# Performance work log

Measured on AMD Instinct MI355X. Metric: run time of the kernel, lower is better.

Reference implementation:

```python
import jax, jax.numpy as jnp
import numpy as np

N, E, D, L, G = 50000, 800000, 128, 3, 64
DIM_OUT = 10
EPS_BN = 1e-5
EPS_AGG = 1e-6


def setup_inputs() -> dict:
    key = jax.random.key(0)
    ks = jax.random.split(key, 10)
    x = jax.random.normal(ks[0], (N, D), jnp.float32)
    edge_attr = jax.random.normal(ks[1], (E, D), jnp.float32)
    edge_index = jax.random.randint(ks[2], (2, E), 0, N)
    batch_vec = jnp.sort(jax.random.randint(ks[3], (N,), 0, G))
    s = 1.0 / np.sqrt(D)
    def w(k, shape):
        return jax.random.uniform(k, shape, jnp.float32, -s, s)
    lin_w = w(ks[4], (L, 4, D, D))   # per-layer stacked A,B,D,E weights
    lin_b = w(ks[5], (L, 4, D))
    bn_gamma = jnp.ones((L, D), jnp.float32)
    bn_beta = jnp.zeros((L, D), jnp.float32)
    post_w1 = w(ks[6], (D, D)); post_b1 = w(ks[7], (D,))
    post_w2 = w(ks[8], (D, DIM_OUT)); post_b2 = w(ks[9], (DIM_OUT,))
    return dict(x=x, edge_attr=edge_attr, edge_index=edge_index, batch_vec=batch_vec,
                lin_w=lin_w, lin_b=lin_b, bn_gamma=bn_gamma, bn_beta=bn_beta,
                post_w1=post_w1, post_b1=post_b1, post_w2=post_w2, post_b2=post_b2)


def _batchnorm_train(h, gamma, beta):
    # training-mode BN over node dim (biased variance, as in torch)
    mu = h.mean(0)
    var = h.var(0)
    return (h - mu) * jax.lax.rsqrt(var + EPS_BN) * gamma + beta


def reference(x, edge_attr, edge_index, batch_vec, lin_w, lin_b, bn_gamma, bn_beta,
              post_w1, post_b1, post_w2, post_b2):
    src, dst = edge_index[0], edge_index[1]   # j -> i (source_to_target)
    e = edge_attr
    for l in range(L):
        x_in = x
        # fused A,B,D,E projections: [4, N, D]
        proj = jnp.einsum('nd,kdo->kno', x, lin_w[l]) + lin_b[l][:, None, :]
        Ax, Bx, Dx, Ex = proj[0], proj[1], proj[2], proj[3]
        e_ij = Dx[dst] + Ex[src]                # [E, D]
        sigma = jax.nn.sigmoid(e_ij)
        num = jax.ops.segment_sum(sigma * Bx[src], dst, num_segments=N)
        den = jax.ops.segment_sum(sigma, dst, num_segments=N)
        h = Ax + num / (den + EPS_AGG)
        h = jax.nn.relu(_batchnorm_train(h, bn_gamma[l], bn_beta[l]))
        x = x_in + h                            # residual
        e = e_ij                                # edge features updated (bn_edge_e unused in forward)
    counts = jax.ops.segment_sum(jnp.ones((N,), x.dtype), batch_vec, num_segments=G)
    pooled = jax.ops.segment_sum(x, batch_vec, num_segments=G) / jnp.maximum(counts, 1.0)[:, None]
    h = jax.nn.relu(pooled @ post_w1 + post_b1)
    return h @ post_w2 + post_b2                # [G, DIM_OUT]
```

## Files before the change

kernel.cpp:

```cpp
#include <hip/hip_runtime.h>
#include <math.h>

constexpr int N_NODES = 50000;
constexpr int N_EDGES = 800000;
constexpr int DIM     = 128;
constexpr int NLAYERS = 3;
constexpr int NGRAPH  = 64;
constexpr int DOUT    = 10;
constexpr float EPS_BN  = 1e-5f;
constexpr float EPS_AGG = 1e-6f;

typedef __attribute__((ext_vector_type(8))) short   bf16x8;
typedef __attribute__((ext_vector_type(4))) float   floatx4;
typedef __attribute__((ext_vector_type(4))) unsigned short ushort4v;

__device__ inline unsigned short f2bf(float f) {
    union { float f; unsigned int u; } v; v.f = f;
    unsigned int u = v.u;
    return (unsigned short)((u + 0x7fffu + ((u >> 16) & 1u)) >> 16);
}
__device__ inline float bf2f(unsigned short h) {
    union { unsigned int u; float f; } v; v.u = ((unsigned int)h) << 16;
    return v.f;
}

__global__ void hist_kernel(const int* __restrict__ dst, int* __restrict__ cnt) {
    int e = blockIdx.x * 256 + threadIdx.x;
    if (e < N_EDGES) atomicAdd(&cnt[dst[e]], 1);
}

__global__ void scan1_kernel(const int* __restrict__ cnt, int* __restrict__ row_ptr,
                             int* __restrict__ partials) {
    __shared__ int s[256];
    int i = blockIdx.x * 256 + threadIdx.x;
    int v = (i < N_NODES) ? cnt[i] : 0;
    s[threadIdx.x] = v;
    __syncthreads();
    for (int off = 1; off < 256; off <<= 1) {
        int t = (threadIdx.x >= off) ? s[threadIdx.x - off] : 0;
        __syncthreads();
        s[threadIdx.x] += t;
        __syncthreads();
    }
    if (i < N_NODES) row_ptr[i] = s[threadIdx.x] - v;
    if (threadIdx.x == 255) partials[blockIdx.x] = s[255];
}

__global__ void scan2_kernel(int* partials, int nb) {
    __shared__ int s[256];
    int t = threadIdx.x;
    int v = (t < nb) ? partials[t] : 0;
    s[t] = v;
    __syncthreads();
    for (int off = 1; off < 256; off <<= 1) {
        int u = (t >= off) ? s[t - off] : 0;
        __syncthreads();
        s[t] += u;
        __syncthreads();
    }
    if (t < nb) partials[t] = s[t] - v;
}

__global__ void scan3_kernel(int* row_ptr, const int* __restrict__ partials) {
    int i = blockIdx.x * 256 + threadIdx.x;
    if (i < N_NODES) row_ptr[i] += partials[blockIdx.x];
    if (blockIdx.x == 0 && threadIdx.x == 0) row_ptr[N_NODES] = N_EDGES;
}

__global__ void scatter_kernel(const int* __restrict__ src, const int* __restrict__ dst,
                               const int* __restrict__ row_ptr, int* __restrict__ cursor,
                               int* __restrict__ col_src) {
    int e = blockIdx.x * 256 + threadIdx.x;
    if (e < N_EDGES) {
        int d = dst[e];
        int pos = row_ptr[d] + atomicAdd(&cursor[d], 1);
        col_src[pos] = src[e];
    }
}

__global__ void wconv_kernel(const float* __restrict__ W, unsigned short* __restrict__ Wt) {
    int idx = blockIdx.x * 256 + threadIdx.x;
    int c = idx & 127, d = (idx >> 7) & 127, lk = idx >> 14;
    Wt[((size_t)lk * 128 + c) * 128 + d] = f2bf(W[idx]);
}

__global__ __launch_bounds__(256) void xinit_kernel(const float* __restrict__ x_in,
                                                    float* __restrict__ x_cur,
                                                    unsigned short* __restrict__ xb) {
    int i4 = blockIdx.x * 256 + threadIdx.x;
    float4 v = *(const float4*)&x_in[(size_t)i4 * 4];
    *(float4*)&x_cur[(size_t)i4 * 4] = v;
    ushort4v b; b.x = f2bf(v.x); b.y = f2bf(v.y); b.z = f2bf(v.z); b.w = f2bf(v.w);
    *(ushort4v*)&xb[(size_t)i4 * 4] = b;
}

__global__ __launch_bounds__(256) void gemm_mfma(const unsigned short* __restrict__ xb,
                                                 const unsigned short* __restrict__ Wt,
                                                 const float* __restrict__ bias,
                                                 float* __restrict__ Axh,
                                                 float* __restrict__ Dx,
                                                 unsigned int* __restrict__ EB) {
    const int ksl = blockIdx.y;
    const int m0  = blockIdx.x * 128;
    const int tid = threadIdx.x;
    const int wave = tid >> 6, lane = tid & 63;
    const int wm = (wave >> 1) * 64, wc = (wave & 1) * 64;
    const int quad = lane >> 4, l16 = lane & 15;
    const unsigned short* Wk = Wt + (size_t)ksl * DIM * DIM;

    floatx4 acc[4][4];
#pragma unroll
    for (int i = 0; i < 4; i++)
#pragma unroll
        for (int j = 0; j < 4; j++) acc[i][j] = (floatx4)0.f;

#pragma unroll
    for (int ks = 0; ks < 4; ks++) {
        const int kk = ks * 32 + quad * 8;
        bf16x8 a[4], b[4];
#pragma unroll
        for (int i = 0; i < 4; i++) {
            int row = m0 + wm + i * 16 + l16;
            row = min(row, N_NODES - 1);
            a[i] = *(const bf16x8*)&xb[(size_t)row * DIM + kk];
        }
#pragma unroll
        for (int j = 0; j < 4; j++) {
            int col = wc + j * 16 + l16;
            b[j] = *(const bf16x8*)&Wk[(size_t)col * DIM + kk];
        }
#pragma unroll
        for (int i = 0; i < 4; i++)
#pragma unroll
            for (int j = 0; j < 4; j++)
                acc[i][j] = __builtin_amdgcn_mfma_f32_16x16x32_bf16(a[i], b[j], acc[i][j], 0, 0, 0);
    }

    float bv[4];
#pragma unroll
    for (int j = 0; j < 4; j++) bv[j] = bias[ksl * DIM + wc + j * 16 + l16];

    float* fdst = (ksl == 0) ? Axh : Dx;
    unsigned short* ebp = (unsigned short*)EB;
    const int half = (ksl == 3) ? 1 : 0;

#pragma unroll
    for (int i = 0; i < 4; i++) {
#pragma unroll
        for (int r = 0; r < 4; r++) {
            int row = m0 + wm + i * 16 + quad * 4 + r;
            if (row >= N_NODES) continue;
            if ((ksl & 1) == 0) {
                float* op = fdst + (size_t)row * DIM;
#pragma unroll
                for (int j = 0; j < 4; j++)
                    op[wc + j * 16 + l16] = acc[i][j][r] + bv[j];
            } else {
                unsigned short* op = ebp + (size_t)row * DIM * 2 + half;
#pragma unroll
                for (int j = 0; j < 4; j++)
                    op[(wc + j * 16 + l16) * 2] = f2bf(acc[i][j][r] + bv[j]);
            }
        }
    }
}

__global__ __launch_bounds__(128) void agg_kernel(float* __restrict__ Axh,
                                                  const float* __restrict__ Dx,
                                                  const unsigned int* __restrict__ EB,
                                                  const int* __restrict__ row_ptr,
                                                  const int* __restrict__ col_src) {
    const int i = blockIdx.x;
    const int d = threadIdx.x;

    const float dx = Dx[(size_t)i * DIM + d];
    float num = 0.f, den = 0.f;
    const int e0 = row_ptr[i], e1 = row_ptr[i + 1];
    int e = e0;
    for (; e + 3 < e1; e += 4) {
        int s0 = col_src[e], s1 = col_src[e + 1];
        int s2 = col_src[e + 2], s3 = col_src[e + 3];
        unsigned int w0 = EB[(size_t)s0 * DIM + d];
        unsigned int w1 = EB[(size_t)s1 * DIM + d];
        unsigned int w2 = EB[(size_t)s2 * DIM + d];
        unsigned int w3 = EB[(size_t)s3 * DIM + d];
        float sg0 = 1.f / (1.f + __expf(-(dx + bf2f((unsigned short)(w0 >> 16)))));
        float sg1 = 1.f / (1.f + __expf(-(dx + bf2f((unsigned short)(w1 >> 16)))));
        float sg2 = 1.f / (1.f + __expf(-(dx + bf2f((unsigned short)(w2 >> 16)))));
        float sg3 = 1.f / (1.f + __expf(-(dx + bf2f((unsigned short)(w3 >> 16)))));
        num += sg0 * bf2f((unsigned short)(w0 & 0xffff))
             + sg1 * bf2f((unsigned short)(w1 & 0xffff))
             + sg2 * bf2f((unsigned short)(w2 & 0xffff))
             + sg3 * bf2f((unsigned short)(w3 & 0xffff));
        den += sg0 + sg1 + sg2 + sg3;
    }
    for (; e < e1; e++) {
        int s = col_src[e];
        unsigned int w = EB[(size_t)s * DIM + d];
        float sg = 1.f / (1.f + __expf(-(dx + bf2f((unsigned short)(w >> 16)))));
        num += sg * bf2f((unsigned short)(w & 0xffff));
        den += sg;
    }
    float ax = Axh[(size_t)i * DIM + d];
    Axh[(size_t)i * DIM + d] = ax + num / (den + EPS_AGG);
}

__global__ __launch_bounds__(256) void bnstat_kernel(const float* __restrict__ h,
                                                     float* __restrict__ bn_sum,
                                                     float* __restrict__ bn_sumsq) {
    __shared__ float ss[256], sq[256];
    int t = threadIdx.x;
    int d = t & 127, half = t >> 7;
    int r0 = blockIdx.x * 256;
    float s = 0.f, q = 0.f;
    for (int r = r0 + half; r < r0 + 256 && r < N_NODES; r += 2) {
        float v = h[(size_t)r * DIM + d];
        s += v; q += v * v;
    }
    ss[t] = s; sq[t] = q;
    __syncthreads();
    if (t < 128) {
        atomicAdd(&bn_sum[d], ss[t] + ss[t + 128]);
        atomicAdd(&bn_sumsq[d], sq[t] + sq[t + 128]);
    }
}

__global__ void bnfin_kernel(const float* __restrict__ bn_sum, const float* __restrict__ bn_sumsq,
                             const float* __restrict__ gamma, const float* __restrict__ beta,
                             float* __restrict__ scale, float* __restrict__ shift) {
    int d = threadIdx.x;
    float mu  = bn_sum[d] * (1.f / N_NODES);
    float var = bn_sumsq[d] * (1.f / N_NODES) - mu * mu;
    float sc  = gamma[d] * rsqrtf(var + EPS_BN);
    scale[d] = sc;
    shift[d] = beta[d] - mu * sc;
}

__global__ __launch_bounds__(256) void apply_kernel(const float* __restrict__ h,
                                                    const float* __restrict__ scale,
                                                    const float* __restrict__ shift,
                                                    float* __restrict__ x,
                                                    unsigned short* __restrict__ xb) {
    int i4 = blockIdx.x * 256 + threadIdx.x;
    int d  = (i4 * 4) & 127;
    float4 hv = *(const float4*)&h[(size_t)i4 * 4];
    float4 xv = *(float4*)&x[(size_t)i4 * 4];
    xv.x += fmaxf(hv.x * scale[d + 0] + shift[d + 0], 0.f);
    xv.y += fmaxf(hv.y * scale[d + 1] + shift[d + 1], 0.f);
    xv.z += fmaxf(hv.z * scale[d + 2] + shift[d + 2], 0.f);
    xv.w += fmaxf(hv.w * scale[d + 3] + shift[d + 3], 0.f);
    *(float4*)&x[(size_t)i4 * 4] = xv;
    ushort4v b; b.x = f2bf(xv.x); b.y = f2bf(xv.y); b.z = f2bf(xv.z); b.w = f2bf(xv.w);
    *(ushort4v*)&xb[(size_t)i4 * 4] = b;
}

__global__ __launch_bounds__(128) void pool_kernel(const float* __restrict__ x,
                                                   const int* __restrict__ batch,
                                                   float* __restrict__ pooled,
                                                   int* __restrict__ gcount) {
    int d = threadIdx.x;
    int r0 = blockIdx.x * 256;
    int r1 = min(r0 + 256, N_NODES);
    int curg = batch[r0];
    float acc = 0.f;
    int run = 0;
    for (int r = r0; r < r1; r++) {
        int g = batch[r];
        if (g != curg) {
            atomicAdd(&pooled[curg * DIM + d], acc);
            if (d == 0) atomicAdd(&gcount[curg], run);
            acc = 0.f; run = 0; curg = g;
        }
        acc += x[(size_t)r * DIM + d];
        run++;
    }
    atomicAdd(&pooled[curg * DIM + d], acc);
    if (d == 0) atomicAdd(&gcount[curg], run);
}

__global__ __launch_bounds__(128) void head_kernel(const float* __restrict__ pooled,
                                                   const int* __restrict__ gcount,
                                                   const float* __restrict__ w1,
                                                   const float* __restrict__ b1,
                                                   const float* __restrict__ w2,
                                                   const float* __restrict__ b2,
                                                   float* __restrict__ out) {
    __shared__ float sp[128], sh[128];
    int g = blockIdx.x, d = threadIdx.x;
    float c = (float)max(gcount[g], 1);
    sp[d] = pooled[g * DIM + d] / c;
    __syncthreads();
    float acc = b1[d];
    for (int dd = 0; dd < DIM; dd++) acc += sp[dd] * w1[dd * DIM + d];
    sh[d] = fmaxf(acc, 0.f);
    __syncthreads();
    if (d < DOUT) {
        float o = b2[d];
        for (int dd = 0; dd < DIM; dd++) o += sh[dd] * w2[dd * DOUT + d];
        out[g * DOUT + d] = o;
    }
}

extern "C" void kernel_launch(void* const* d_in, const int* in_sizes, int n_in,
                              void* d_out, int out_size, void* d_ws, size_t ws_size,
                              hipStream_t stream) {
    const float* x_in  = (const float*)d_in[0];
    const int*   eidx  = (const int*)d_in[2];
    const int*   batch = (const int*)d_in[3];
    const float* lin_w = (const float*)d_in[4];
    const float* lin_b = (const float*)d_in[5];
    const float* gamma = (const float*)d_in[6];
    const float* beta  = (const float*)d_in[7];
    const float* w1    = (const float*)d_in[8];
    const float* b1    = (const float*)d_in[9];
    const float* w2    = (const float*)d_in[10];
    const float* b2    = (const float*)d_in[11];
    float* out = (float*)d_out;

    const int* src = eidx;
    const int* dst = eidx + N_EDGES;

    auto al = [](size_t v) { return (v + 255) & ~(size_t)255; };
    size_t off = 0;
    size_t o_xcur = off; off = al(off + (size_t)N_NODES * DIM * 4);
    size_t o_xb   = off; off = al(off + (size_t)N_NODES * DIM * 2);
    size_t o_wt   = off; off = al(off + (size_t)NLAYERS * 4 * DIM * DIM * 2);
    size_t o_axh  = off; off = al(off + (size_t)N_NODES * DIM * 4);
    size_t o_dx   = off; off = al(off + (size_t)N_NODES * DIM * 4);
    size_t o_eb   = off; off = al(off + (size_t)N_NODES * DIM * 4);
    size_t o_rp   = off; off = al(off + (size_t)(N_NODES + 1) * 4);
    size_t o_cs   = off; off = al(off + (size_t)N_EDGES * 4);
    size_t o_cnt  = off; off = al(off + (size_t)N_NODES * 4);
    size_t o_part = off; off = al(off + 256 * 4);
    size_t o_bn   = off; off = al(off + 512 * 4);
    size_t o_pool = off; off = al(off + (size_t)NGRAPH * DIM * 4);
    size_t o_gc   = off; off = al(off + (size_t)NGRAPH * 4);
    size_t total  = off;

    char* base = (ws_size >= total) ? (char*)d_ws : (char*)d_in[1];

    float*          x_cur    = (float*)(base + o_xcur);
    unsigned short* xb       = (unsigned short*)(base + o_xb);
    unsigned short* Wt       = (unsigned short*)(base + o_wt);
    float*          Axh      = (float*)(base + o_axh);
    float*          Dx       = (float*)(base + o_dx);
    unsigned int*   EB       = (unsigned int*)(base + o_eb);
    int*            row_ptr  = (int*)  (base + o_rp);
    int*            col_src  = (int*)  (base + o_cs);
    int*            cnt      = (int*)  (base + o_cnt);
    int*            partials = (int*)  (base + o_part);
    float*          bn_sum   = (float*)(base + o_bn);
    float*          bn_sumsq = bn_sum + 128;
    float*          bn_scale = bn_sum + 256;
    float*          bn_shift = bn_sum + 384;
    float*          pooled   = (float*)(base + o_pool);
    int*            gcount   = (int*)  (base + o_gc);

    const int nbN = (N_NODES + 255) / 256;
    const int nbE = (N_EDGES + 255) / 256;
    const int nb4 = (N_NODES * DIM / 4) / 256;

    xinit_kernel<<<nb4, 256, 0, stream>>>(x_in, x_cur, xb);
    wconv_kernel<<<(NLAYERS * 4 * DIM * DIM) / 256, 256, 0, stream>>>(lin_w, Wt);

    hipMemsetAsync(cnt, 0, (size_t)N_NODES * 4, stream);
    hist_kernel<<<nbE, 256, 0, stream>>>(dst, cnt);
    scan1_kernel<<<nbN, 256, 0, stream>>>(cnt, row_ptr, partials);
    scan2_kernel<<<1, 256, 0, stream>>>(partials, nbN);
    scan3_kernel<<<nbN, 256, 0, stream>>>(row_ptr, partials);
    hipMemsetAsync(cnt, 0, (size_t)N_NODES * 4, stream);
    scatter_kernel<<<nbE, 256, 0, stream>>>(src, dst, row_ptr, cnt, col_src);

    for (int l = 0; l < NLAYERS; l++) {
        gemm_mfma<<<dim3((N_NODES + 127) / 128, 4), 256, 0, stream>>>(
            xb, Wt + (size_t)l * 4 * DIM * DIM, lin_b + (size_t)l * 4 * DIM, Axh, Dx, EB);
        agg_kernel<<<N_NODES, 128, 0, stream>>>(Axh, Dx, EB, row_ptr, col_src);
        hipMemsetAsync(bn_sum, 0, 256 * 4, stream);
        bnstat_kernel<<<nbN, 256, 0, stream>>>(Axh, bn_sum, bn_sumsq);
        bnfin_kernel<<<1, 128, 0, stream>>>(bn_sum, bn_sumsq, gamma + l * DIM, beta + l * DIM,
                                            bn_scale, bn_shift);
        apply_kernel<<<nb4, 256, 0, stream>>>(Axh, bn_scale, bn_shift, x_cur, xb);
    }

    hipMemsetAsync(pooled, 0, (size_t)NGRAPH * DIM * 4, stream);
    hipMemsetAsync(gcount, 0, (size_t)NGRAPH * 4, stream);
    pool_kernel<<<nbN, 128, 0, stream>>>(x_cur, batch, pooled, gcount);
    head_kernel<<<NGRAPH, 128, 0, stream>>>(pooled, gcount, w1, b1, w2, b2, out);
}
```

Measured before the change: 1.124 ms.

## Fuse BN statistics into aggregation and BN finalize into apply kernel

The aggregation kernel now processes 8 nodes per 128-thread slot with two slots per block. It gathers 8 edges at a time with masked tail handling and accumulates per-feature sum and sum-of-squares, which it atomically adds into 8 striped partial buffers. The separate bnstat, bnfin and memset launches are removed. The GEMM zeroes the partial buffers and the apply kernel reduces them into scale/shift in shared memory. This cuts launches and one full read of h per layer, and spreads atomic contention over 8 buckets. The cost is less parallelism per block for high-degree nodes and a redundant finalize in every apply block.

Result: no change. 1.143 ms (+1.7%).

```diff
diff --git a/kernel.cpp b/kernel.cpp
--- a/kernel.cpp
+++ b/kernel.cpp
@@ -99,10 +99,17 @@
                                                  const float* __restrict__ bias,
                                                  float* __restrict__ Axh,
                                                  float* __restrict__ Dx,
-                                                 unsigned int* __restrict__ EB) {
+                                                 unsigned int* __restrict__ EB,
+                                                 float* __restrict__ bn8) {
     const int ksl = blockIdx.y;
     const int m0  = blockIdx.x * 128;
     const int tid = threadIdx.x;
+
+    if (blockIdx.x == 0 && ksl == 0) {
+#pragma unroll
+        for (int c = 0; c < 8; c++) bn8[c * 256 + tid] = 0.f;
+    }
+
     const int wave = tid >> 6, lane = tid & 63;
     const int wm = (wave >> 1) * 64, wc = (wave & 1) * 64;
     const int quad = lane >> 4, l16 = lane & 15;
@@ -165,90 +172,90 @@
     }
 }
 
-__global__ __launch_bounds__(128) void agg_kernel(float* __restrict__ Axh,
+__global__ __launch_bounds__(256) void agg_kernel(float* __restrict__ Axh,
                                                   const float* __restrict__ Dx,
                                                   const unsigned int* __restrict__ EB,
                                                   const int* __restrict__ row_ptr,
-                                                  const int* __restrict__ col_src) {
-    const int i = blockIdx.x;
-    const int d = threadIdx.x;
-
-    const float dx = Dx[(size_t)i * DIM + d];
-    float num = 0.f, den = 0.f;
-    const int e0 = row_ptr[i], e1 = row_ptr[i + 1];
-    int e = e0;
-    for (; e + 3 < e1; e += 4) {
-        int s0 = col_src[e], s1 = col_src[e + 1];
-        int s2 = col_src[e + 2], s3 = col_src[e + 3];
-        unsigned int w0 = EB[(size_t)s0 * DIM + d];
-        unsigned int w1 = EB[(size_t)s1 * DIM + d];
-        unsigned int w2 = EB[(size_t)s2 * DIM + d];
-        unsigned int w3 = EB[(size_t)s3 * DIM + d];
-        float sg0 = 1.f / (1.f + __expf(-(dx + bf2f((unsigned short)(w0 >> 16)))));
-        float sg1 = 1.f / (1.f + __expf(-(dx + bf2f((unsigned short)(w1 >> 16)))));
-        float sg2 = 1.f / (1.f + __expf(-(dx + bf2f((unsigned short)(w2 >> 16)))));
-        float sg3 = 1.f / (1.f + __expf(-(dx + bf2f((unsigned short)(w3 >> 16)))));
-        num += sg0 * bf2f((unsigned short)(w0 & 0xffff))
-             + sg1 * bf2f((unsigned short)(w1 & 0xffff))
-             + sg2 * bf2f((unsigned short)(w2 & 0xffff))
-             + sg3 * bf2f((unsigned short)(w3 & 0xffff));
-        den += sg0 + sg1 + sg2 + sg3;
-    }
-    for (; e < e1; e++) {
-        int s = col_src[e];
-        unsigned int w = EB[(size_t)s * DIM + d];
-        float sg = 1.f / (1.f + __expf(-(dx + bf2f((unsigned short)(w >> 16)))));
-        num += sg * bf2f((unsigned short)(w & 0xffff));
-        den += sg;
-    }
-    float ax = Axh[(size_t)i * DIM + d];
-    Axh[(size_t)i * DIM + d] = ax + num / (den + EPS_AGG);
-}
-
-__global__ __launch_bounds__(256) void bnstat_kernel(const float* __restrict__ h,
-                                                     float* __restrict__ bn_sum,
-                                                     float* __restrict__ bn_sumsq) {
-    __shared__ float ss[256], sq[256];
-    int t = threadIdx.x;
-    int d = t & 127, half = t >> 7;
-    int r0 = blockIdx.x * 256;
-    float s = 0.f, q = 0.f;
-    for (int r = r0 + half; r < r0 + 256 && r < N_NODES; r += 2) {
-        float v = h[(size_t)r * DIM + d];
-        s += v; q += v * v;
-    }
-    ss[t] = s; sq[t] = q;
-    __syncthreads();
-    if (t < 128) {
-        atomicAdd(&bn_sum[d], ss[t] + ss[t + 128]);
-        atomicAdd(&bn_sumsq[d], sq[t] + sq[t + 128]);
-    }
-}
-
-__global__ void bnfin_kernel(const float* __restrict__ bn_sum, const float* __restrict__ bn_sumsq,
-                             const float* __restrict__ gamma, const float* __restrict__ beta,
-                             float* __restrict__ scale, float* __restrict__ shift) {
-    int d = threadIdx.x;
-    float mu  = bn_sum[d] * (1.f / N_NODES);
-    float var = bn_sumsq[d] * (1.f / N_NODES) - mu * mu;
-    float sc  = gamma[d] * rsqrtf(var + EPS_BN);
-    scale[d] = sc;
-    shift[d] = beta[d] - mu * sc;
+                                                  const int* __restrict__ col_src,
+                                                  float* __restrict__ bn8) {
+    const int slot = threadIdx.x >> 7;
+    const int d    = threadIdx.x & 127;
+    const int i0   = (blockIdx.x * 2 + slot) * 8;
+
+    float s_acc = 0.f, q_acc = 0.f;
+
+#pragma unroll 1
+    for (int n = 0; n < 8; n++) {
+        const int i = i0 + n;
+        const float ax = Axh[(size_t)i * DIM + d];
+        const float dx = Dx[(size_t)i * DIM + d];
+        const int e0 = row_ptr[i];
+        const int e1 = row_ptr[i + 1];
+        float num = 0.f, den = 0.f;
+        const int nr = (e1 - e0 + 7) >> 3;
+#pragma unroll 1
+        for (int r = 0; r < nr; r++) {
+            const int eb = e0 + r * 8;
+            int idx[8];
+#pragma unroll
+            for (int k = 0; k < 8; k++) idx[k] = col_src[min(eb + k, e1 - 1)];
+            unsigned int w[8];
+#pragma unroll
+            for (int k = 0; k < 8; k++) w[k] = EB[(size_t)idx[k] * DIM + d];
+#pragma unroll
+            for (int k = 0; k < 8; k++) {
+                float ex = bf2f((unsigned short)(w[k] >> 16));
+                float bx = bf2f((unsigned short)(w[k] & 0xffffu));
+                float sg = 1.f / (1.f + __expf(-(dx + ex)));
+                sg = (eb + k < e1) ? sg : 0.f;
+                num += sg * bx;
+                den += sg;
+            }
+        }
+        const float h = ax + num / (den + EPS_AGG);
+        Axh[(size_t)i * DIM + d] = h;
+        s_acc += h;
+        q_acc += h * h;
+    }
+
+    __shared__ float ls[256], lq[256];
+    ls[threadIdx.x] = s_acc; lq[threadIdx.x] = q_acc;
+    __syncthreads();
+    if (threadIdx.x < 128) {
+        float* bp = bn8 + (blockIdx.x & 7) * 256;
+        atomicAdd(&bp[d],       ls[threadIdx.x] + ls[threadIdx.x + 128]);
+        atomicAdd(&bp[128 + d], lq[threadIdx.x] + lq[threadIdx.x + 128]);
+    }
 }
 
 __global__ __launch_bounds__(256) void apply_kernel(const float* __restrict__ h,
-                                                    const float* __restrict__ scale,
-                                                    const float* __restrict__ shift,
+                                                    const float* __restrict__ bn8,
+                                                    const float* __restrict__ gamma,
+                                                    const float* __restrict__ beta,
                                                     float* __restrict__ x,
                                                     unsigned short* __restrict__ xb) {
-    int i4 = blockIdx.x * 256 + threadIdx.x;
+    __shared__ float ssc[128], ssh[128];
+    const int t = threadIdx.x;
+    if (t < 128) {
+        float s = 0.f, q = 0.f;
+#pragma unroll
+        for (int c = 0; c < 8; c++) { s += bn8[c * 256 + t]; q += bn8[c * 256 + 128 + t]; }
+        const float mu  = s * (1.f / N_NODES);
+        const float var = q * (1.f / N_NODES) - mu * mu;
+        const float sc  = gamma[t] * rsqrtf(var + EPS_BN);
+        ssc[t] = sc;
+        ssh[t] = beta[t] - mu * sc;
+    }
+    __syncthreads();
+
+    int i4 = blockIdx.x * 256 + t;
     int d  = (i4 * 4) & 127;
     float4 hv = *(const float4*)&h[(size_t)i4 * 4];
     float4 xv = *(float4*)&x[(size_t)i4 * 4];
-    xv.x += fmaxf(hv.x * scale[d + 0] + shift[d + 0], 0.f);
-    xv.y += fmaxf(hv.y * scale[d + 1] + shift[d + 1], 0.f);
-    xv.z += fmaxf(hv.z * scale[d + 2] + shift[d + 2], 0.f);
-    xv.w += fmaxf(hv.w * scale[d + 3] + shift[d + 3], 0.f);
+    xv.x += fmaxf(hv.x * ssc[d + 0] + ssh[d + 0], 0.f);
+    xv.y += fmaxf(hv.y * ssc[d + 1] + ssh[d + 1], 0.f);
+    xv.z += fmaxf(hv.z * ssc[d + 2] + ssh[d + 2], 0.f);
+    xv.w += fmaxf(hv.w * ssc[d + 3] + ssh[d + 3], 0.f);
     *(float4*)&x[(size_t)i4 * 4] = xv;
     ushort4v b; b.x = f2bf(xv.x); b.y = f2bf(xv.y); b.z = f2bf(xv.z); b.w = f2bf(xv.w);
     *(ushort4v*)&xb[(size_t)i4 * 4] = b;
@@ -332,7 +339,7 @@
     size_t o_cs   = off; off = al(off + (size_t)N_EDGES * 4);
     size_t o_cnt  = off; off = al(off + (size_t)N_NODES * 4);
     size_t o_part = off; off = al(off + 256 * 4);
-    size_t o_bn   = off; off = al(off + 512 * 4);
+    size_t o_bn   = off; off = al(off + 2048 * 4);
     size_t o_pool = off; off = al(off + (size_t)NGRAPH * DIM * 4);
     size_t o_gc   = off; off = al(off + (size_t)NGRAPH * 4);
     size_t total  = off;
@@ -349,16 +356,14 @@
     int*            col_src  = (int*)  (base + o_cs);
     int*            cnt      = (int*)  (base + o_cnt);
     int*            partials = (int*)  (base + o_part);
-    float*          bn_sum   = (float*)(base + o_bn);
-    float*          bn_sumsq = bn_sum + 128;
-    float*          bn_scale = bn_sum + 256;
-    float*          bn_shift = bn_sum + 384;
+    float*          bn8      = (float*)(base + o_bn);
     float*          pooled   = (float*)(base + o_pool);
     int*            gcount   = (int*)  (base + o_gc);
 
     const int nbN = (N_NODES + 255) / 256;
     const int nbE = (N_EDGES + 255) / 256;
     const int nb4 = (N_NODES * DIM / 4) / 256;
+    const int nbAgg = N_NODES / 16;
 
     xinit_kernel<<<nb4, 256, 0, stream>>>(x_in, x_cur, xb);
     wconv_kernel<<<(NLAYERS * 4 * DIM * DIM) / 256, 256, 0, stream>>>(lin_w, Wt);
@@ -373,13 +378,10 @@
 
     for (int l = 0; l < NLAYERS; l++) {
         gemm_mfma<<<dim3((N_NODES + 127) / 128, 4), 256, 0, stream>>>(
-            xb, Wt + (size_t)l * 4 * DIM * DIM, lin_b + (size_t)l * 4 * DIM, Axh, Dx, EB);
-        agg_kernel<<<N_NODES, 128, 0, stream>>>(Axh, Dx, EB, row_ptr, col_src);
-        hipMemsetAsync(bn_sum, 0, 256 * 4, stream);
-        bnstat_kernel<<<nbN, 256, 0, stream>>>(Axh, bn_sum, bn_sumsq);
-        bnfin_kernel<<<1, 128, 0, stream>>>(bn_sum, bn_sumsq, gamma + l * DIM, beta + l * DIM,
-                                            bn_scale, bn_shift);
-        apply_kernel<<<nb4, 256, 0, stream>>>(Axh, bn_scale, bn_shift, x_cur, xb);
+            xb, Wt + (size_t)l * 4 * DIM * DIM, lin_b + (size_t)l * 4 * DIM, Axh, Dx, EB, bn8);
+        agg_kernel<<<nbAgg, 256, 0, stream>>>(Axh, Dx, EB, row_ptr, col_src, bn8);
+        apply_kernel<<<nb4, 256, 0, stream>>>(Axh, bn8, gamma + (size_t)l * DIM,
+                                              beta + (size_t)l * DIM, x_cur, xb);
     }
 
     hipMemsetAsync(pooled, 0, (size_t)NGRAPH * DIM * 4, stream);
```
